# Optimization experiments

Hardware: AMD Instinct MI355X
Metric: run time of the kernel (lower is better)

## Reference

```python
import jax, jax.numpy as jnp
import numpy as np

H = 16        # n_heads
D = 1024      # d_model
SPLIT = 4     # number of sequence blocks, each with its own MHA weights
DK = D // H   # head dim
B = 4
SEQ = 4096


def setup_inputs() -> dict:
    key = jax.random.key(0)
    ks = jax.random.split(key, 9)
    sc = 1.0 / np.sqrt(D).astype(np.float32)
    x = jax.random.normal(ks[0], (B, SEQ, D), jnp.float32)
    # Per-split projection weights (torch Linear applied as x @ W + b; random init so
    # the transpose convention is immaterial for a correctness baseline).
    Wq = jax.random.normal(ks[1], (SPLIT, D, D), jnp.float32) * sc
    Wk = jax.random.normal(ks[2], (SPLIT, D, D), jnp.float32) * sc
    Wv = jax.random.normal(ks[3], (SPLIT, D, D), jnp.float32) * sc
    Wo = jax.random.normal(ks[4], (SPLIT, D, D), jnp.float32) * sc
    bq = jax.random.normal(ks[5], (SPLIT, D), jnp.float32) * 0.02
    bk = jax.random.normal(ks[6], (SPLIT, D), jnp.float32) * 0.02
    bv = jax.random.normal(ks[7], (SPLIT, D), jnp.float32) * 0.02
    bo = jax.random.normal(ks[8], (SPLIT, D), jnp.float32) * 0.02
    return {"x": x, "Wq": Wq, "Wk": Wk, "Wv": Wv, "Wo": Wo,
            "bq": bq, "bk": bk, "bv": bv, "bo": bo}


def reference(x, Wq, Wk, Wv, Wo, bq, bk, bv, bo):
    b, l, d = x.shape
    L = l // SPLIT                     # block length
    xs = x.reshape(b, SPLIT, L, d)     # [b, s, L, d] block-diagonal structure

    def proj(W, bias):
        return jnp.einsum('bsld,sde->bsle', xs, W) + bias[None, :, None, :]

    q = proj(Wq, bq).reshape(b, SPLIT, L, H, DK)
    k = proj(Wk, bk).reshape(b, SPLIT, L, H, DK)
    v = proj(Wv, bv).reshape(b, SPLIT, L, H, DK)

    # scaled dot-product attention within each block, causal mask per block
    scores = jnp.einsum('bslhk,bsmhk->bshlm', q, k) / np.sqrt(DK).astype(np.float32)
    causal = jnp.tril(jnp.ones((L, L), dtype=bool))
    scores = jnp.where(causal[None, None, None], scores, jnp.float32(-1e9))
    attn = jax.nn.softmax(scores, axis=-1)   # dropout is identity in eval mode
    o = jnp.einsum('bshlm,bsmhk->bslhk', attn, v).reshape(b, SPLIT, L, d)

    out = jnp.einsum('bsld,sde->bsle', o, Wo) + bo[None, :, None, :]
    return out.reshape(b, l, d)
```

## Files before the change

kernel.cpp:

```cpp
#include <hip/hip_runtime.h>
#include <stdint.h>

#define H_ 16
#define D_ 1024
#define SPLIT_ 4
#define DK_ 64
#define B_ 4
#define SEQ_ 4096
#define L_ 1024

#define QSC 0.18033688f

typedef unsigned short ushort_t;
typedef __attribute__((ext_vector_type(8))) short short8;
typedef __attribute__((ext_vector_type(4))) float floatx4;
typedef __attribute__((ext_vector_type(4))) unsigned short ushortx4;

__device__ __forceinline__ ushort_t f2bf(float f) {
  union { float f; unsigned u; } cv; cv.f = f;
  unsigned u = cv.u;
  return (ushort_t)((u + 0x7fffu + ((u >> 16) & 1u)) >> 16);
}

__device__ __forceinline__ uint32_t pack_bf_trunc(float x, float y) {
#if __has_builtin(__builtin_amdgcn_perm)
  return __builtin_amdgcn_perm(__float_as_uint(y), __float_as_uint(x), 0x07060302u);
#else
  return (__float_as_uint(y) & 0xffff0000u) | (__float_as_uint(x) >> 16);
#endif
}

__device__ __forceinline__ float exp2f_fast(float x) {
#if __has_builtin(__builtin_amdgcn_exp2f)
  return __builtin_amdgcn_exp2f(x);
#else
  return exp2f(x);
#endif
}

__device__ __forceinline__ void gl2lds16(const ushort_t* g, ushort_t* l) {
  __builtin_amdgcn_global_load_lds(
      (const __attribute__((address_space(1))) uint32_t*)g,
      (__attribute__((address_space(3))) uint32_t*)l, 16, 0, 0);
}

__global__ __launch_bounds__(256) void convert_x(const float* __restrict__ X,
                                                 ushort_t* __restrict__ Y) {
  const int i = blockIdx.x * 256 + threadIdx.x;
  const float4 v = ((const float4*)X)[i];
  ushortx4 o;
  o[0] = f2bf(v.x); o[1] = f2bf(v.y); o[2] = f2bf(v.z); o[3] = f2bf(v.w);
  ((ushortx4*)Y)[i] = o;
}

__global__ __launch_bounds__(256) void wt_convert_all(const float* __restrict__ W0,
                                                      const float* __restrict__ W1,
                                                      const float* __restrict__ W2,
                                                      const float* __restrict__ W3,
                                                      ushort_t* __restrict__ Wt) {
  __shared__ ushort_t tile[32][33];
  const int z = blockIdx.z, mat = z >> 2, s = z & 3;
  const float* W = (mat == 0) ? W0 : (mat == 1) ? W1 : (mat == 2) ? W2 : W3;
  const float scale = (mat == 0) ? QSC : 1.0f;
  const float* Ws = W + (size_t)s * D_ * D_;
  ushort_t* Wts = Wt + ((size_t)mat * SPLIT_ + s) * D_ * D_;
  const int e0 = blockIdx.x * 32, d0 = blockIdx.y * 32;
  for (int i = threadIdx.y; i < 32; i += 8)
    tile[i][threadIdx.x] = f2bf(Ws[(size_t)(d0 + i) * D_ + e0 + threadIdx.x] * scale);
  __syncthreads();
  for (int i = threadIdx.y; i < 32; i += 8)
    Wts[(size_t)(e0 + i) * D_ + d0 + threadIdx.x] = tile[threadIdx.x][i];
}

template <int MODE>
__global__ __launch_bounds__(256) void gemm_bt(const ushort_t* __restrict__ X,
                                               const ushort_t* __restrict__ Wt,
                                               const float* __restrict__ bias,
                                               float bscale,
                                               void* __restrict__ Cv) {
  __shared__ __attribute__((aligned(16))) ushort_t SH[8192];
  ushort_t* As = SH;
  ushort_t* Bs = SH + 4096;

  const int xcd = blockIdx.x;
  const int u = blockIdx.y;
  const int bs = xcd + ((u >> 6) << 3);
  const int mn = u & 63;
  const int m0 = (mn >> 3) * 128;
  const int n0 = (mn & 7) * 128;
  const int s = bs & 3;
  const ushort_t* Xb = X + (size_t)bs * (L_ * D_);
  const ushort_t* Wts = Wt + (size_t)s * (D_ * D_);

  const int t = threadIdx.x;
  const int lane = t & 63;
  const int w = t >> 6;
  const int wm = w >> 1, wn = w & 1;
  const int quad = lane >> 4, cl = lane & 15;

  floatx4 acc[4][4];
  floatx4 zero = {0.f, 0.f, 0.f, 0.f};
#pragma unroll
  for (int i = 0; i < 4; ++i)
#pragma unroll
    for (int j = 0; j < 4; ++j) acc[i][j] = zero;

  const int c0 = t, c1 = t + 256;
  const int r0 = c0 >> 2, cc0 = ((c0 & 3) ^ (r0 & 3)) * 8;
  const int r1 = c1 >> 2, cc1 = ((c1 & 3) ^ (r1 & 3)) * 8;
  const int sw = (quad ^ (cl & 3)) * 8;

  for (int k0 = 0; k0 < D_; k0 += 32) {
    gl2lds16(Xb + (size_t)(m0 + r0) * D_ + k0 + cc0, &As[c0 * 8]);
    gl2lds16(Xb + (size_t)(m0 + r1) * D_ + k0 + cc1, &As[c1 * 8]);
    gl2lds16(Wts + (size_t)(n0 + r0) * D_ + k0 + cc0, &Bs[c0 * 8]);
    gl2lds16(Wts + (size_t)(n0 + r1) * D_ + k0 + cc1, &Bs[c1 * 8]);
    __syncthreads();
    short8 a[4], b[4];
#pragma unroll
    for (int i = 0; i < 4; ++i)
      a[i] = *(const short8*)&As[(wm * 64 + i * 16 + cl) * 32 + sw];
#pragma unroll
    for (int j = 0; j < 4; ++j)
      b[j] = *(const short8*)&Bs[(wn * 64 + j * 16 + cl) * 32 + sw];
#pragma unroll
    for (int i = 0; i < 4; ++i)
#pragma unroll
      for (int j = 0; j < 4; ++j)
        acc[i][j] = __builtin_amdgcn_mfma_f32_16x16x32_bf16(a[i], b[j], acc[i][j], 0, 0, 0);
    __syncthreads();
  }

  float bvj[4];
#pragma unroll
  for (int j = 0; j < 4; ++j)
    bvj[j] = bias[s * D_ + n0 + wn * 64 + j * 16 + cl] * bscale;

  if (MODE == 2) {
#pragma unroll
    for (int j = 0; j < 4; ++j) {
      const int col = n0 + wn * 64 + j * 16 + cl;
#pragma unroll
      for (int i = 0; i < 4; ++i) {
        const int rb = m0 + wm * 64 + i * 16 + quad * 4;
        float* Cf = (float*)Cv + (size_t)bs * (L_ * D_) + (size_t)rb * D_ + col;
#pragma unroll
        for (int r = 0; r < 4; ++r) Cf[(size_t)r * D_] = acc[i][j][r] + bvj[j];
      }
    }
    return;
  }

  ushort_t* CT = SH;
#pragma unroll
  for (int ph = 0; ph < 2; ++ph) {
    __syncthreads();
    if (MODE == 0 ? (wm == ph) : (wn == ph)) {
#pragma unroll
      for (int i = 0; i < 4; ++i)
#pragma unroll
        for (int j = 0; j < 4; ++j)
#pragma unroll
          for (int r = 0; r < 4; ++r) {
            int row, col;
            if (MODE == 0) { row = i * 16 + quad * 4 + r; col = wn * 64 + j * 16 + cl; }
            else           { row = j * 16 + cl;           col = wm * 64 + i * 16 + quad * 4 + r; }
            const int ch = col >> 3, off = col & 7;
            CT[row * 128 + ((ch ^ (row & 15)) << 3) + off] = f2bf(acc[i][j][r] + bvj[j]);
          }
    }
    __syncthreads();
#pragma unroll
    for (int pass = 0; pass < 4; ++pass) {
      const int row = pass * 16 + (t >> 4);
      const int ck = t & 15;
      const short8 v = *(const short8*)&CT[row * 128 + ((ck ^ (row & 15)) << 3)];
      if (MODE == 0) {
        *(short8*)((ushort_t*)Cv + (size_t)bs * (L_ * D_) +
                   (size_t)(m0 + ph * 64 + row) * D_ + n0 + ck * 8) = v;
      } else {
        *(short8*)((ushort_t*)Cv + (size_t)bs * (L_ * D_) +
                   (size_t)(n0 + ph * 64 + row) * L_ + m0 + ck * 8) = v;
      }
    }
  }
}

__device__ __forceinline__ void attn_step(const ushort_t* __restrict__ Kbuf,
                                          const ushort_t* __restrict__ Vbuf,
                                          ushort_t* __restrict__ PTw,
                                          const short8 qa0, const short8 qa1,
                                          floatx4 (&o)[4], float& m_i, float& l_i,
                                          const bool diag, const int w,
                                          const int quad, const int cl) {
  floatx4 zero = {0.f, 0.f, 0.f, 0.f};
  const int sw0 = (quad ^ (cl & 7)) * 8;
  const int sw1 = ((4 + quad) ^ (cl & 7)) * 8;

  floatx4 st[4];
#pragma unroll
  for (int j = 0; j < 4; ++j) {
    const int row = (j * 16 + cl) * 64;
    const short8 ka0 = *(const short8*)&Kbuf[row + sw0];
    const short8 ka1 = *(const short8*)&Kbuf[row + sw1];
    floatx4 z = zero;
    z = __builtin_amdgcn_mfma_f32_16x16x32_bf16(ka0, qa0, z, 0, 0, 0);
    z = __builtin_amdgcn_mfma_f32_16x16x32_bf16(ka1, qa1, z, 0, 0, 0);
    st[j] = z;
  }

  if (diag) {
    const int ql = w * 16 + cl;
#pragma unroll
    for (int j = 0; j < 4; ++j)
#pragma unroll
      for (int r = 0; r < 4; ++r)
        if (j * 16 + quad * 4 + r > ql) st[j][r] = -1e30f;
  }

  float tm = fmaxf(fmaxf(fmaxf(st[0][0], st[0][1]), fmaxf(st[0][2], st[0][3])),
                   fmaxf(fmaxf(st[1][0], st[1][1]), fmaxf(st[1][2], st[1][3])));
  tm = fmaxf(tm, fmaxf(fmaxf(fmaxf(st[2][0], st[2][1]), fmaxf(st[2][2], st[2][3])),
                       fmaxf(fmaxf(st[3][0], st[3][1]), fmaxf(st[3][2], st[3][3]))));
  tm = fmaxf(tm, __shfl_xor(tm, 16, 64));
  tm = fmaxf(tm, __shfl_xor(tm, 32, 64));
  const float mnew = fmaxf(m_i, tm);
  const float alpha = exp2f_fast(m_i - mnew);
  m_i = mnew;

  float tsv = 0.f;
#pragma unroll
  for (int j = 0; j < 4; ++j)
#pragma unroll
    for (int r = 0; r < 4; ++r) {
      st[j][r] = exp2f_fast(st[j][r] - mnew);
      tsv += st[j][r];
    }
  tsv += __shfl_xor(tsv, 16, 64);
  tsv += __shfl_xor(tsv, 32, 64);
  l_i = l_i * alpha + tsv;

#pragma unroll
  for (int j = 0; j < 4; ++j) {
    const int base = cl * 72 + j * 16 + quad * 4;
    *(uint32_t*)&PTw[base] = pack_bf_trunc(st[j][0], st[j][1]);
    *(uint32_t*)&PTw[base + 2] = pack_bf_trunc(st[j][2], st[j][3]);
  }

#pragma unroll
  for (int j = 0; j < 4; ++j)
#pragma unroll
    for (int r = 0; r < 4; ++r) o[j][r] *= alpha;

  const short8 pb0 = *(const short8*)&PTw[cl * 72 + quad * 8];
  const short8 pb1 = *(const short8*)&PTw[cl * 72 + 32 + quad * 8];
#pragma unroll
  for (int j = 0; j < 4; ++j) {
    const int row = (j * 16 + cl) * 64;
    const short8 va0 = *(const short8*)&Vbuf[row + sw0];
    const short8 va1 = *(const short8*)&Vbuf[row + sw1];
    o[j] = __builtin_amdgcn_mfma_f32_16x16x32_bf16(va0, pb0, o[j], 0, 0, 0);
    o[j] = __builtin_amdgcn_mfma_f32_16x16x32_bf16(va1, pb1, o[j], 0, 0, 0);
  }
}

__device__ __forceinline__ void attn_store(ushort_t* __restrict__ O, size_t act_base,
                                           int qt, int h, const floatx4 (&o)[4],
                                           float l_i, int w, int quad, int cl) {
  const float inv = 1.0f / l_i;
  ushort_t* Orow = O + act_base + (size_t)(qt * 64 + w * 16 + cl) * D_ + h * DK_;
#pragma unroll
  for (int j = 0; j < 4; ++j) {
    ushortx4 pk;
#pragma unroll
    for (int r = 0; r < 4; ++r) pk[r] = f2bf(o[j][r] * inv);
    *(ushortx4*)(Orow + j * 16 + quad * 4) = pk;
  }
}

__global__ __launch_bounds__(256) void attn_kernel(const ushort_t* __restrict__ Q,
                                                   const ushort_t* __restrict__ K,
                                                   const ushort_t* __restrict__ Vt,
                                                   ushort_t* __restrict__ O) {
  __shared__ __attribute__((aligned(16))) ushort_t Ks[2][64 * 64];
  __shared__ __attribute__((aligned(16))) ushort_t Vts[2][64 * 64];
  __shared__ __attribute__((aligned(16))) ushort_t PT[8][1152];

  const int p = blockIdx.x, h = blockIdx.y, bs = blockIdx.z;
  const int t = threadIdx.x, lane = t & 63, w = t >> 6;
  const int quad = lane >> 4, cl = lane & 15;
  const size_t act_base = (size_t)bs * (L_ * D_);
  const int qtA = p, qtB = 15 - p;
  const int NIT = 16 - p;

  const int cA = t, cB = t + 256;
  const int rA = cA >> 3, ccA = ((cA & 7) ^ (rA & 7)) * 8;
  const int rB = cB >> 3, ccB = ((cB & 7) ^ (rB & 7)) * 8;

  const ushort_t* pKA = K + act_base + (size_t)rA * D_ + h * DK_ + ccA;
  const ushort_t* pKB = K + act_base + (size_t)rB * D_ + h * DK_ + ccB;
  const ushort_t* pVA = Vt + act_base + (size_t)(h * DK_ + rA) * L_ + ccA;
  const ushort_t* pVB = Vt + act_base + (size_t)(h * DK_ + rB) * L_ + ccB;
  const size_t kstep = (size_t)64 * D_, vstep = 64;

  floatx4 zero = {0.f, 0.f, 0.f, 0.f};

  const ushort_t* QpA = Q + act_base + (size_t)(qtA * 64 + w * 16 + cl) * D_ + h * DK_ + quad * 8;
  const ushort_t* QpB = Q + act_base + (size_t)(qtB * 64 + w * 16 + cl) * D_ + h * DK_ + quad * 8;
  const short8 qaA0 = *(const short8*)QpA;
  const short8 qaA1 = *(const short8*)(QpA + 32);
  const short8 qaB0 = *(const short8*)QpB;
  const short8 qaB1 = *(const short8*)(QpB + 32);

  floatx4 oA[4], oB[4];
#pragma unroll
  for (int j = 0; j < 4; ++j) { oA[j] = zero; oB[j] = zero; }
  float mA = -3.0e38f, lA = 0.f, mB = -3.0e38f, lB = 0.f;

  gl2lds16(pKA, &Ks[0][cA * 8]);
  gl2lds16(pKB, &Ks[0][cB * 8]);
  gl2lds16(pVA, &Vts[0][cA * 8]);
  gl2lds16(pVB, &Vts[0][cB * 8]);

  for (int kv = 0; kv < NIT; ++kv) {
    __syncthreads();
    if (kv + 1 < NIT) {
      pKA += kstep; pKB += kstep; pVA += vstep; pVB += vstep;
      const int nb = (kv + 1) & 1;
      gl2lds16(pKA, &Ks[nb][cA * 8]);
      gl2lds16(pKB, &Ks[nb][cB * 8]);
      gl2lds16(pVA, &Vts[nb][cA * 8]);
      gl2lds16(pVB, &Vts[nb][cB * 8]);
    }
    const int buf = kv & 1;

    if (kv <= p) {
      attn_step(Ks[buf], Vts[buf], PT[w], qaA0, qaA1, oA, mA, lA,
                kv == p, w, quad, cl);
      if (kv == p) attn_store(O, act_base, qtA, h, oA, lA, w, quad, cl);
    }
    attn_step(Ks[buf], Vts[buf], PT[w + 4], qaB0, qaB1, oB, mB, lB,
              kv == NIT - 1, w, quad, cl);
  }
  attn_store(O, act_base, qtB, h, oB, lB, w, quad, cl);
}

extern "C" void kernel_launch(void* const* d_in, const int* in_sizes, int n_in,
                              void* d_out, int out_size, void* d_ws, size_t ws_size,
                              hipStream_t stream) {
  const float* x  = (const float*)d_in[0];
  const float* Wq = (const float*)d_in[1];
  const float* Wk = (const float*)d_in[2];
  const float* Wv = (const float*)d_in[3];
  const float* Wo = (const float*)d_in[4];
  const float* bq = (const float*)d_in[5];
  const float* bk = (const float*)d_in[6];
  const float* bv = (const float*)d_in[7];
  const float* bo = (const float*)d_in[8];

  const size_t WT_SZ = (size_t)SPLIT_ * D_ * D_;
  const size_t ACT_SZ = (size_t)B_ * SEQ_ * D_;

  ushort_t* ws0 = (ushort_t*)d_ws;
  ushort_t* xbf = ws0;
  ushort_t* wtall = xbf + ACT_SZ;
  ushort_t* wtq = wtall;
  ushort_t* wtk = wtq + WT_SZ;
  ushort_t* wtv = wtk + WT_SZ;
  ushort_t* wto = wtv + WT_SZ;
  ushort_t* Vtb = wto + WT_SZ;
  ushort_t* Qb = (ushort_t*)d_out;
  ushort_t* Kb = Qb + ACT_SZ;
  ushort_t* Ob = xbf;

  convert_x<<<ACT_SZ / 1024, 256, 0, stream>>>(x, xbf);
  wt_convert_all<<<dim3(32, 32, 16), dim3(32, 8, 1), 0, stream>>>(Wq, Wk, Wv, Wo, wtall);

  dim3 gb(256, 1, 1), gg(8, 128, 1);
  gemm_bt<0><<<gg, gb, 0, stream>>>(xbf, wtq, bq, QSC, Qb);
  gemm_bt<0><<<gg, gb, 0, stream>>>(xbf, wtk, bk, 1.0f, Kb);
  gemm_bt<1><<<gg, gb, 0, stream>>>(xbf, wtv, bv, 1.0f, Vtb);

  dim3 ag(8, 16, 16);
  attn_kernel<<<ag, dim3(256, 1, 1), 0, stream>>>(Qb, Kb, Vtb, Ob);

  gemm_bt<2><<<gg, gb, 0, stream>>>(Ob, wto, bo, 1.0f, d_out);
}
```

Before: 469.0 us.

## Fuse Q, K, V projections into one GEMM kernel sharing the X tile

Replaces three separate projection GEMM launches with one kernel that stages each X tile once and multiplies it against the Q, K and V weight tiles together (128x64 output tile per matrix). This cuts repeated reads of the activation tile and two kernel launches. In exchange it uses more LDS and accumulator registers per block, which may lower occupancy, and the N tile is narrower.

Result: faster. 453.3 us (-3.3%).

```diff
diff --git a/kernel.cpp b/kernel.cpp
--- a/kernel.cpp
+++ b/kernel.cpp
@@ -42,6 +42,12 @@
   __builtin_amdgcn_global_load_lds(
       (const __attribute__((address_space(1))) uint32_t*)g,
       (__attribute__((address_space(3))) uint32_t*)l, 16, 0, 0);
+}
+
+__device__ __forceinline__ void wave_barrier() {
+  asm volatile("" ::: "memory");
+  __builtin_amdgcn_s_barrier();
+  asm volatile("" ::: "memory");
 }
 
 __global__ __launch_bounds__(256) void convert_x(const float* __restrict__ X,
@@ -72,6 +78,152 @@
     Wts[(size_t)(e0 + i) * D_ + d0 + threadIdx.x] = tile[threadIdx.x][i];
 }
 
+__global__ __launch_bounds__(256) void gemm_qkv(const ushort_t* __restrict__ X,
+                                                const ushort_t* __restrict__ Wt,
+                                                const float* __restrict__ Bq,
+                                                const float* __restrict__ Bk,
+                                                const float* __restrict__ Bv,
+                                                ushort_t* __restrict__ Qo,
+                                                ushort_t* __restrict__ Ko,
+                                                ushort_t* __restrict__ Vo) {
+  __shared__ __attribute__((aligned(16))) ushort_t SH[20480];
+
+  const size_t WT = (size_t)D_ * D_;
+  const int xcd = blockIdx.x;
+  const int u = blockIdx.y;
+  const int bs = xcd + ((u >> 7) << 3);
+  const int mn = u & 127;
+  const int m0 = (mn >> 4) * 128;
+  const int n0 = (mn & 15) * 64;
+  const int s = bs & 3;
+  const ushort_t* Xb = X + (size_t)bs * (L_ * D_);
+
+  const int t = threadIdx.x;
+  const int lane = t & 63;
+  const int w = t >> 6;
+  const int wm = w >> 1, wn = w & 1;
+  const int quad = lane >> 4, cl = lane & 15;
+  const int sw = (quad ^ (cl & 3)) * 8;
+
+  floatx4 acc[3][4][2];
+  floatx4 zero = {0.f, 0.f, 0.f, 0.f};
+#pragma unroll
+  for (int mt = 0; mt < 3; ++mt)
+#pragma unroll
+    for (int i = 0; i < 4; ++i)
+#pragma unroll
+      for (int j = 0; j < 2; ++j) acc[mt][i][j] = zero;
+
+  const int c0 = t, c1 = t + 256;
+  const int r0 = c0 >> 2, cc0 = ((c0 & 3) ^ (r0 & 3)) * 8;
+  const int r1 = c1 >> 2, cc1 = ((c1 & 3) ^ (r1 & 3)) * 8;
+  const ushort_t* A0 = Xb + (size_t)(m0 + r0) * D_ + cc0;
+  const ushort_t* A1 = Xb + (size_t)(m0 + r1) * D_ + cc1;
+  const ushort_t* Bsrc0 = Wt + (0 * SPLIT_ + s) * WT + (size_t)(n0 + r0) * D_ + cc0;
+  const ushort_t* Bsrc1 = Wt + (1 * SPLIT_ + s) * WT + (size_t)(n0 + r0) * D_ + cc0;
+  const ushort_t* Bsrc2 = Wt + (2 * SPLIT_ + s) * WT + (size_t)(n0 + r0) * D_ + cc0;
+
+  auto STAGE = [&](int buf, int k0) {
+    gl2lds16(A0 + k0, &SH[buf * 4096 + c0 * 8]);
+    gl2lds16(A1 + k0, &SH[buf * 4096 + c1 * 8]);
+    gl2lds16(Bsrc0 + k0, &SH[8192 + buf * 6144 + 0 * 2048 + t * 8]);
+    gl2lds16(Bsrc1 + k0, &SH[8192 + buf * 6144 + 1 * 2048 + t * 8]);
+    gl2lds16(Bsrc2 + k0, &SH[8192 + buf * 6144 + 2 * 2048 + t * 8]);
+  };
+
+  auto COMPUTE = [&](int buf) {
+    const ushort_t* Ab = &SH[buf * 4096];
+    const ushort_t* Bb = &SH[8192 + buf * 6144];
+    short8 a[4];
+#pragma unroll
+    for (int i = 0; i < 4; ++i)
+      a[i] = *(const short8*)&Ab[(wm * 64 + i * 16 + cl) * 32 + sw];
+#pragma unroll
+    for (int mt = 0; mt < 3; ++mt) {
+      const ushort_t* Bm = Bb + mt * 2048;
+      const short8 b0 = *(const short8*)&Bm[(wn * 32 + cl) * 32 + sw];
+      const short8 b1 = *(const short8*)&Bm[(wn * 32 + 16 + cl) * 32 + sw];
+#pragma unroll
+      for (int i = 0; i < 4; ++i) {
+        acc[mt][i][0] = __builtin_amdgcn_mfma_f32_16x16x32_bf16(a[i], b0, acc[mt][i][0], 0, 0, 0);
+        acc[mt][i][1] = __builtin_amdgcn_mfma_f32_16x16x32_bf16(a[i], b1, acc[mt][i][1], 0, 0, 0);
+      }
+    }
+  };
+
+  STAGE(0, 0);
+  for (int kt = 0; kt < 31; ++kt) {
+    STAGE((kt + 1) & 1, (kt + 1) * 32);
+    asm volatile("s_waitcnt vmcnt(5)" ::: "memory");
+    wave_barrier();
+    COMPUTE(kt & 1);
+    wave_barrier();
+  }
+  asm volatile("s_waitcnt vmcnt(0)" ::: "memory");
+  wave_barrier();
+  COMPUTE(1);
+
+  __syncthreads();
+  ushort_t* CT = SH;
+
+#pragma unroll
+  for (int mt = 0; mt < 2; ++mt) {
+    const float* bp = (mt == 0) ? Bq : Bk;
+    ushort_t* Og = (mt == 0) ? Qo : Ko;
+    const float bscale = (mt == 0) ? QSC : 1.0f;
+    float bvj[2];
+#pragma unroll
+    for (int j = 0; j < 2; ++j)
+      bvj[j] = bp[s * D_ + n0 + wn * 32 + j * 16 + cl] * bscale;
+#pragma unroll
+    for (int i = 0; i < 4; ++i)
+#pragma unroll
+      for (int j = 0; j < 2; ++j)
+#pragma unroll
+        for (int r = 0; r < 4; ++r) {
+          const int row = wm * 64 + i * 16 + quad * 4 + r;
+          const int col = wn * 32 + j * 16 + cl;
+          const int ch = col >> 3, off = col & 7;
+          CT[row * 64 + ((ch ^ (row & 7)) << 3) + off] = f2bf(acc[mt][i][j][r] + bvj[j]);
+        }
+    __syncthreads();
+#pragma unroll
+    for (int pass = 0; pass < 4; ++pass) {
+      const int row = pass * 32 + (t >> 3);
+      const int ck = t & 7;
+      const short8 v = *(const short8*)&CT[row * 64 + ((ck ^ (row & 7)) << 3)];
+      *(short8*)(Og + (size_t)bs * (L_ * D_) + (size_t)(m0 + row) * D_ + n0 + ck * 8) = v;
+    }
+    __syncthreads();
+  }
+
+  {
+    float bvj[2];
+#pragma unroll
+    for (int j = 0; j < 2; ++j)
+      bvj[j] = Bv[s * D_ + n0 + wn * 32 + j * 16 + cl];
+#pragma unroll
+    for (int i = 0; i < 4; ++i)
+#pragma unroll
+      for (int j = 0; j < 2; ++j)
+#pragma unroll
+        for (int r = 0; r < 4; ++r) {
+          const int row = wn * 32 + j * 16 + cl;
+          const int col = wm * 64 + i * 16 + quad * 4 + r;
+          const int ch = col >> 3, off = col & 7;
+          CT[row * 128 + ((ch ^ (row & 15)) << 3) + off] = f2bf(acc[2][i][j][r] + bvj[j]);
+        }
+    __syncthreads();
+#pragma unroll
+    for (int pass = 0; pass < 4; ++pass) {
+      const int row = pass * 16 + (t >> 4);
+      const int ck = t & 15;
+      const short8 v = *(const short8*)&CT[row * 128 + ((ck ^ (row & 15)) << 3)];
+      *(short8*)(Vo + (size_t)bs * (L_ * D_) + (size_t)(n0 + row) * L_ + m0 + ck * 8) = v;
+    }
+  }
+}
+
 template <int MODE>
 __global__ __launch_bounds__(256) void gemm_bt(const ushort_t* __restrict__ X,
                                                const ushort_t* __restrict__ Wt,
@@ -364,11 +516,8 @@
   ushort_t* ws0 = (ushort_t*)d_ws;
   ushort_t* xbf = ws0;
   ushort_t* wtall = xbf + ACT_SZ;
-  ushort_t* wtq = wtall;
-  ushort_t* wtk = wtq + WT_SZ;
-  ushort_t* wtv = wtk + WT_SZ;
-  ushort_t* wto = wtv + WT_SZ;
-  ushort_t* Vtb = wto + WT_SZ;
+  ushort_t* wto = wtall + 3 * WT_SZ;
+  ushort_t* Vtb = wtall + 4 * WT_SZ;
   ushort_t* Qb = (ushort_t*)d_out;
   ushort_t* Kb = Qb + ACT_SZ;
   ushort_t* Ob = xbf;
@@ -376,13 +525,11 @@
   convert_x<<<ACT_SZ / 1024, 256, 0, stream>>>(x, xbf);
   wt_convert_all<<<dim3(32, 32, 16), dim3(32, 8, 1), 0, stream>>>(Wq, Wk, Wv, Wo, wtall);
 
-  dim3 gb(256, 1, 1), gg(8, 128, 1);
-  gemm_bt<0><<<gg, gb, 0, stream>>>(xbf, wtq, bq, QSC, Qb);
-  gemm_bt<0><<<gg, gb, 0, stream>>>(xbf, wtk, bk, 1.0f, Kb);
-  gemm_bt<1><<<gg, gb, 0, stream>>>(xbf, wtv, bv, 1.0f, Vtb);
+  gemm_qkv<<<dim3(8, 256, 1), dim3(256, 1, 1), 0, stream>>>(
+      xbf, wtall, bq, bk, bv, Qb, Kb, Vtb);
 
   dim3 ag(8, 16, 16);
   attn_kernel<<<ag, dim3(256, 1, 1), 0, stream>>>(Qb, Kb, Vtb, Ob);
 
-  gemm_bt<2><<<gg, gb, 0, stream>>>(Ob, wto, bo, 1.0f, d_out);
-}
+  gemm_bt<2><<<dim3(8, 128, 1), dim3(256, 1, 1), 0, stream>>>(Ob, wto, bo, 1.0f, d_out);
+}
```
